# Optimization experiments

Hardware: AMD Instinct MI355X
Metric: run time of the kernel (lower is better)

The kernel has to match this reference:

```python
import jax, jax.numpy as jnp
import numpy as np

B, T_IN, T_OUT, C = 32, 512, 256, 64
NB_IN, NB_OUT = 16, 16
D = 128          # d_model
L = 3            # e_layers (hidden Siren layers before last)
E_IN = NB_IN * C
E_OUT = NB_OUT * C
LIN_IN = (NB_IN + 1) * C + 4
LIN_OUT = (NB_OUT + 1) * C


def _siren_params(key, E, w0_initial):
    ks = jax.random.split(key, 6)
    def unif(k, shape, std):
        return jax.random.uniform(k, shape, jnp.float32, -std, std)
    c6 = float(np.sqrt(6.0 / D))
    return dict(
        W0=unif(ks[0], (E, D, 1), 1.0),        # first layer: w_std = 1/dim_in, dim_in=1
        b0=unif(ks[1], (E, D), 1.0),
        Wh=unif(ks[2], (L - 1, E, D, D), c6),   # sqrt(6/dim)/w0, w0=1
        bh=unif(ks[3], (L - 1, E, D), c6),
        Wl=unif(ks[4], (E, 1, D), c6),
        bl=unif(ks[5], (E, 1), c6),
        w0i=w0_initial,                          # per-ensemble first-layer frequency
    )


def setup_inputs() -> dict:
    key = jax.random.key(0)
    ks = jax.random.split(key, 8)
    inp = {
        "x_enc": jax.random.normal(ks[0], (B, T_IN, C), jnp.float32),
        "x_mark_enc": jax.random.normal(ks[1], (B, T_IN, 4), jnp.float32),
        "x_dec": jax.random.normal(ks[2], (B, T_OUT, C), jnp.float32),
        "x_mark_dec": jax.random.normal(ks[3], (B, T_OUT, 4), jnp.float32),
    }
    # w0_initial: repeat(linspace(1, nb, nb), 'e -> (e c)')
    w0i_in = jnp.repeat(jnp.linspace(1.0, NB_IN, NB_IN, dtype=jnp.float32), C)
    w0i_out = jnp.repeat(jnp.linspace(1.0, NB_OUT, NB_OUT, dtype=jnp.float32), C)
    p_in = _siren_params(ks[4], E_IN, w0i_in)
    p_out = _siren_params(ks[5], E_OUT, w0i_out)
    for k, v in p_in.items():
        inp[k + "_in"] = v
    for k, v in p_out.items():
        inp[k + "_out"] = v
    std = float(1.0 / np.sqrt(LIN_IN))
    inp["Wlin"] = jax.random.uniform(ks[6], (LIN_OUT, LIN_IN), jnp.float32, -std, std)
    inp["blin"] = jax.random.uniform(ks[7], (LIN_OUT,), jnp.float32, -std, std)
    return inp


def _eigenfunc(T, nb, W0, b0, Wh, bh, Wl, bl, w0i):
    # SirenNet on domain [T,1] -> normalized eigenfunctions [T, nb+1, C]
    domain = jnp.linspace(0.0, 1.0, T, dtype=W0.dtype)[:, None]
    y = jnp.einsum('eoi,ti->teo', W0, domain) + b0           # [T,E,D]
    x = jnp.sin(w0i[None, :, None] * y)                       # Sine(w0_initial)
    for l in range(Wh.shape[0]):                              # hidden layers, w0 = 1
        x = jnp.sin(jnp.einsum('eoi,tei->teo', Wh[l], x) + bh[l])
    y = jnp.einsum('eoi,tei->teo', Wl, x) + bl                # [T,E,1], identity final act
    ef = y.reshape(T, nb, C)                                  # 't (e c) 1 -> t e c'
    ef = jnp.concatenate([jnp.ones((T, 1, C), ef.dtype), ef], axis=1)  # add_ones
    norm = jnp.sqrt(jnp.sum(ef * ef, axis=1, keepdims=True))  # normalize over basis dim
    return ef / norm


def reference(x_enc, x_mark_enc, x_dec, x_mark_dec,
              W0_in, b0_in, Wh_in, bh_in, Wl_in, bl_in, w0i_in,
              W0_out, b0_out, Wh_out, bh_out, Wl_out, bl_out, w0i_out,
              Wlin, blin):
    ef_in = _eigenfunc(T_IN, NB_IN, W0_in, b0_in, Wh_in, bh_in, Wl_in, bl_in, w0i_in)
    ef_out = _eigenfunc(T_OUT, NB_OUT, W0_out, b0_out, Wh_out, bh_out, Wl_out, bl_out, w0i_out)
    coeffs = jnp.einsum('btc,tec->bec', x_enc, ef_in)         # [B, nb+1, C]
    label = x_mark_enc[:, -1]                                  # [B, 4]
    flat = coeffs.reshape(coeffs.shape[0], -1)                 # 'b e c -> b (e c)'
    flat_in = jnp.concatenate([flat, label], axis=-1)
    pred = flat_in @ Wlin.T + blin                             # nn.Linear
    pred_coeff = pred.reshape(-1, NB_OUT + 1, C)
    pred_recon = jnp.einsum('bec,tec->btc', pred_coeff, ef_out)  # [B, pred_len, C]
    return pred_recon
```

## Files before the change

### kernel.cpp

```cpp
#include <hip/hip_runtime.h>
#include <hip/hip_bf16.h>
#include <math.h>


typedef short  bf16x8 __attribute__((ext_vector_type(8)));
typedef float  f32x4  __attribute__((ext_vector_type(4)));
typedef unsigned short u16;
typedef u16    u16x8  __attribute__((ext_vector_type(8)));
typedef unsigned int u32;
typedef u32    u32x4  __attribute__((ext_vector_type(4)));

constexpr int DD    = 128;
constexpr int E_TOT = 1024;
constexpr int T_INc = 512;
constexpr int T_OUTc= 256;
constexpr int BBc   = 32;
constexpr int CCc   = 64;
constexpr int NB1   = 17;
constexpr int EF_W  = NB1 * CCc;
constexpr int LIN_I = EF_W + 4;
constexpr int LIN_O = EF_W;

__device__ __forceinline__ u16 f2b(float f) {
  unsigned u = __builtin_bit_cast(unsigned, f);
  return (u16)((u + 0x7FFFu + ((u >> 16) & 1u)) >> 16);
}
__device__ __forceinline__ float b2f(u16 u) {
  unsigned v = ((unsigned)u) << 16;
  return __builtin_bit_cast(float, v);
}
__device__ __forceinline__ u32 pkrn(float a, float b) {
  __hip_bfloat162 h = __float22bfloat162_rn(float2{a, b});
  u32 r;
  __builtin_memcpy(&r, &h, 4);
  return r;
}

__device__ __forceinline__ int swz(int row, int col) {
  return row * DD + ((((col << 1) ^ ((row & 15) << 4)) >> 1));
}

__global__ __launch_bounds__(512, 4) void eigen_persist(
    const float* __restrict__ W0i, const float* __restrict__ b0i,
    const float* __restrict__ Whi, const float* __restrict__ bhi,
    const float* __restrict__ Wli, const float* __restrict__ bli,
    const float* __restrict__ w0ii, float* __restrict__ efni,
    const float* __restrict__ W0o, const float* __restrict__ b0o,
    const float* __restrict__ Who, const float* __restrict__ bho,
    const float* __restrict__ Wlo, const float* __restrict__ blo,
    const float* __restrict__ w0io, float* __restrict__ efno)
{
  __shared__ u16 xP[2][8192];
  __shared__ float w0s[128], b0s[128], wls[128];

  const bool isIn = (blockIdx.x < E_TOT);
  const int  e    = blockIdx.x & (E_TOT - 1);
  const int  NIT  = isIn ? (T_INc / 64) : (T_OUTc / 64);
  const float tstep = isIn ? (1.0f / (float)(T_INc - 1)) : (1.0f / (float)(T_OUTc - 1));
  const float* W0 = isIn ? W0i : W0o;
  const float* b0 = isIn ? b0i : b0o;
  const float* Wh = isIn ? Whi : Who;
  const float* bh = isIn ? bhi : bho;
  const float* Wl = isIn ? Wli : Wlo;
  const float* bl = isIn ? bli : blo;
  const float* w0i = isIn ? w0ii : w0io;
  float* efn = isIn ? efni : efno;

  const int tid  = threadIdx.x;
  const int lane = tid & 63;
  const int wv   = tid >> 6;
  const int wt   = wv >> 2;
  const int wo   = wv & 3;
  const int lm   = lane & 15;
  const int lg   = lane >> 4;

  if (tid < 128)       w0s[tid]       = W0[(size_t)e * DD + tid];
  else if (tid < 256)  b0s[tid - 128] = b0[(size_t)e * DD + tid - 128];
  else if (tid < 384)  wls[tid - 256] = Wl[(size_t)e * DD + tid - 256];
  const float wi  = w0i[e];
  const float blv = bl[e];

  float bhv[2][2];
  #pragma unroll
  for (int l = 0; l < 2; ++l)
    #pragma unroll
    for (int n = 0; n < 2; ++n)
      bhv[l][n] = bh[((size_t)l * E_TOT + e) * DD + wo * 32 + n * 16 + lm];

  bf16x8 wfrag[2][4][2];
  #pragma unroll
  for (int l = 0; l < 2; ++l) {
    const float* Wg = Wh + ((size_t)l * E_TOT + e) * (DD * DD);
    #pragma unroll
    for (int kk = 0; kk < 4; ++kk)
      #pragma unroll
      for (int n = 0; n < 2; ++n) {
        const float* p = Wg + (wo * 32 + n * 16 + lm) * DD + kk * 32 + lg * 8;
        const float4 a = *(const float4*)p;
        const float4 c = *(const float4*)(p + 4);
        u32x4 u;
        u[0] = pkrn(a.x, a.y);
        u[1] = pkrn(a.z, a.w);
        u[2] = pkrn(c.x, c.y);
        u[3] = pkrn(c.z, c.w);
        wfrag[l][kk][n] = __builtin_bit_cast(bf16x8, u);
      }
  }
  __syncthreads();

  const int tl = tid >> 3;
  const int q  = tid & 7;

  for (int it = 0; it < NIT; ++it) {
    u16* pCur = xP[it & 1];
    u16* pAlt = xP[(it & 1) ^ 1];

    {
      const float dom = (float)(it * 64 + tl) * tstep;
      #pragma unroll
      for (int c = 0; c < 2; ++c) {
        const int d = q * 16 + c * 8;
        const float4 wa = *(const float4*)&w0s[d];
        const float4 wb = *(const float4*)&w0s[d + 4];
        const float4 ba = *(const float4*)&b0s[d];
        const float4 bb = *(const float4*)&b0s[d + 4];
        u32x4 u;
        u[0] = pkrn(__sinf(wi * (wa.x * dom + ba.x)), __sinf(wi * (wa.y * dom + ba.y)));
        u[1] = pkrn(__sinf(wi * (wa.z * dom + ba.z)), __sinf(wi * (wa.w * dom + ba.w)));
        u[2] = pkrn(__sinf(wi * (wb.x * dom + bb.x)), __sinf(wi * (wb.y * dom + bb.y)));
        u[3] = pkrn(__sinf(wi * (wb.z * dom + bb.z)), __sinf(wi * (wb.w * dom + bb.w)));
        *(u16x8*)&pCur[swz(tl, d)] = __builtin_bit_cast(u16x8, u);
      }
    }
    __syncthreads();

    f32x4 acc[2][2];

    #pragma unroll
    for (int m = 0; m < 2; ++m)
      #pragma unroll
      for (int n = 0; n < 2; ++n) acc[m][n] = (f32x4){0.f, 0.f, 0.f, 0.f};
    #pragma unroll
    for (int kk = 0; kk < 4; ++kk) {
      const int kb = kk * 32 + lg * 8;
      bf16x8 ah[2];
      #pragma unroll
      for (int m = 0; m < 2; ++m)
        ah[m] = *(const bf16x8*)&pCur[swz(wt * 32 + m * 16 + lm, kb)];
      #pragma unroll
      for (int m = 0; m < 2; ++m)
        #pragma unroll
        for (int n = 0; n < 2; ++n)
          acc[m][n] = __builtin_amdgcn_mfma_f32_16x16x32_bf16(ah[m], wfrag[0][kk][n], acc[m][n], 0, 0, 0);
    }
    #pragma unroll
    for (int m = 0; m < 2; ++m)
      #pragma unroll
      for (int n = 0; n < 2; ++n) {
        const int o = wo * 32 + n * 16 + lm;
        const int t = wt * 32 + m * 16 + lg * 4;
        const u32 p0 = pkrn(__sinf(acc[m][n][0] + bhv[0][n]), __sinf(acc[m][n][1] + bhv[0][n]));
        const u32 p1 = pkrn(__sinf(acc[m][n][2] + bhv[0][n]), __sinf(acc[m][n][3] + bhv[0][n]));
        pAlt[swz(t + 0, o)] = (u16)p0;
        pAlt[swz(t + 1, o)] = (u16)(p0 >> 16);
        pAlt[swz(t + 2, o)] = (u16)p1;
        pAlt[swz(t + 3, o)] = (u16)(p1 >> 16);
      }
    __syncthreads();

    #pragma unroll
    for (int m = 0; m < 2; ++m)
      #pragma unroll
      for (int n = 0; n < 2; ++n) acc[m][n] = (f32x4){0.f, 0.f, 0.f, 0.f};
    #pragma unroll
    for (int kk = 0; kk < 4; ++kk) {
      const int kb = kk * 32 + lg * 8;
      bf16x8 ah[2];
      #pragma unroll
      for (int m = 0; m < 2; ++m)
        ah[m] = *(const bf16x8*)&pAlt[swz(wt * 32 + m * 16 + lm, kb)];
      #pragma unroll
      for (int m = 0; m < 2; ++m)
        #pragma unroll
        for (int n = 0; n < 2; ++n)
          acc[m][n] = __builtin_amdgcn_mfma_f32_16x16x32_bf16(ah[m], wfrag[1][kk][n], acc[m][n], 0, 0, 0);
    }
    #pragma unroll
    for (int m = 0; m < 2; ++m)
      #pragma unroll
      for (int n = 0; n < 2; ++n) {
        const int o = wo * 32 + n * 16 + lm;
        const int t = wt * 32 + m * 16 + lg * 4;
        const u32 p0 = pkrn(__sinf(acc[m][n][0] + bhv[1][n]), __sinf(acc[m][n][1] + bhv[1][n]));
        const u32 p1 = pkrn(__sinf(acc[m][n][2] + bhv[1][n]), __sinf(acc[m][n][3] + bhv[1][n]));
        pCur[swz(t + 0, o)] = (u16)p0;
        pCur[swz(t + 1, o)] = (u16)(p0 >> 16);
        pCur[swz(t + 2, o)] = (u16)p1;
        pCur[swz(t + 3, o)] = (u16)(p1 >> 16);
      }
    __syncthreads();

    {
      const int i = q * 16;
      float a = 0.0f;
      const bf16x8 h0 = *(const bf16x8*)&pCur[swz(tl, i)];
      const bf16x8 h1 = *(const bf16x8*)&pCur[swz(tl, i + 8)];
      const float4 wl0 = *(const float4*)&wls[i];
      const float4 wl1 = *(const float4*)&wls[i + 4];
      const float4 wl2 = *(const float4*)&wls[i + 8];
      const float4 wl3 = *(const float4*)&wls[i + 12];
      a += wl0.x * b2f((u16)h0[0]) + wl0.y * b2f((u16)h0[1])
         + wl0.z * b2f((u16)h0[2]) + wl0.w * b2f((u16)h0[3]);
      a += wl1.x * b2f((u16)h0[4]) + wl1.y * b2f((u16)h0[5])
         + wl1.z * b2f((u16)h0[6]) + wl1.w * b2f((u16)h0[7]);
      a += wl2.x * b2f((u16)h1[0]) + wl2.y * b2f((u16)h1[1])
         + wl2.z * b2f((u16)h1[2]) + wl2.w * b2f((u16)h1[3]);
      a += wl3.x * b2f((u16)h1[4]) + wl3.y * b2f((u16)h1[5])
         + wl3.z * b2f((u16)h1[6]) + wl3.w * b2f((u16)h1[7]);
      a += __shfl_xor(a, 1);
      a += __shfl_xor(a, 2);
      a += __shfl_xor(a, 4);
      if (q == 0)
        efn[(size_t)(it * 64 + tl) * EF_W + CCc + e] = a + blv;
    }
  }
}

__global__ void normalize_kernel(float* __restrict__ efn)
{
  const int t = blockIdx.x;
  const int c = threadIdx.x;
  float* row = efn + (size_t)t * EF_W;
  float v[16];
  float s = 1.0f;
  #pragma unroll
  for (int n = 0; n < 16; ++n) {
    v[n] = row[CCc + n * CCc + c];
    s += v[n] * v[n];
  }
  const float inv = 1.0f / sqrtf(s);
  row[c] = inv;
  #pragma unroll
  for (int n = 0; n < 16; ++n)
    row[CCc + n * CCc + c] = v[n] * inv;
}

__global__ __launch_bounds__(512) void coeffs_kernel(
    const float* __restrict__ x_enc, const float* __restrict__ x_mark_enc,
    const float* __restrict__ efn_in, float* __restrict__ flat_in)
{
  const int n  = blockIdx.x;
  const int b  = blockIdx.y;
  const int c  = threadIdx.x & 63;
  const int ch = threadIdx.x >> 6;
  __shared__ float red[8][64];
  float acc = 0.0f;
  #pragma unroll 4
  for (int t = ch * 64; t < ch * 64 + 64; ++t)
    acc += x_enc[((size_t)b * T_INc + t) * CCc + c]
         * efn_in[(size_t)t * EF_W + n * CCc + c];
  red[ch][c] = acc;
  __syncthreads();
  if (ch == 0) {
    #pragma unroll
    for (int k = 1; k < 8; ++k) acc += red[k][c];
    flat_in[b * LIN_I + n * CCc + c] = acc;
    if (n == 0 && c < 4)
      flat_in[b * LIN_I + EF_W + c] =
          x_mark_enc[((size_t)b * T_INc + (T_INc - 1)) * 4 + c];
  }
}

__global__ __launch_bounds__(256) void transpose_lin(const float* __restrict__ W,
                                                     float* __restrict__ Wt)
{
  __shared__ float tile[32][33];
  const int j0 = blockIdx.x * 32;
  const int o0 = blockIdx.y * 32;
  const int tx = threadIdx.x & 31, ty = threadIdx.x >> 5;
  #pragma unroll
  for (int r = 0; r < 32; r += 8) {
    const int o = o0 + ty + r, j = j0 + tx;
    tile[ty + r][tx] = (o < LIN_O && j < LIN_I) ? W[(size_t)o * LIN_I + j] : 0.f;
  }
  __syncthreads();
  #pragma unroll
  for (int r = 0; r < 32; r += 8) {
    const int j = j0 + ty + r, o = o0 + tx;
    if (j < LIN_I && o < LIN_O) Wt[(size_t)j * LIN_O + o] = tile[tx][ty + r];
  }
}

__global__ __launch_bounds__(256) void linear_t_kernel(
    const float* __restrict__ flat_in, const float* __restrict__ Wt,
    const float* __restrict__ blin, float* __restrict__ pred)
{
  const int og = blockIdx.x;
  const int b  = blockIdx.y;
  const int c  = threadIdx.x & 63;
  const int ch = threadIdx.x >> 6;
  const int o  = og * 64 + c;
  __shared__ float red[4][64];
  const float* xi = flat_in + b * LIN_I;
  float acc = 0.0f;
  #pragma unroll 4
  for (int j = ch * 273; j < ch * 273 + 273; ++j)
    acc += Wt[(size_t)j * LIN_O + o] * xi[j];
  red[ch][c] = acc;
  __syncthreads();
  if (ch == 0)
    pred[b * LIN_O + o] = acc + red[1][c] + red[2][c] + red[3][c] + blin[o];
}

__global__ void linear_row_kernel(const float* __restrict__ flat_in,
                                  const float* __restrict__ Wlin,
                                  const float* __restrict__ blin,
                                  float* __restrict__ pred)
{
  const int o = blockIdx.x * 64 + threadIdx.x;
  const int b = blockIdx.y;
  const float* w  = Wlin + (size_t)o * LIN_I;
  const float* xi = flat_in + b * LIN_I;
  float acc = blin[o];
  for (int j = 0; j < LIN_I; ++j) acc += w[j] * xi[j];
  pred[b * LIN_O + o] = acc;
}

__global__ void recon_kernel(const float* __restrict__ pred,
                             const float* __restrict__ efn_out,
                             float* __restrict__ out)
{
  const int b = blockIdx.y;
  const int t = blockIdx.x * 4 + (threadIdx.x >> 6);
  const int c = threadIdx.x & 63;
  float acc = 0.0f;
  #pragma unroll
  for (int n = 0; n < NB1; ++n)
    acc += pred[b * LIN_O + n * CCc + c]
         * efn_out[(size_t)t * EF_W + n * CCc + c];
  out[((size_t)b * T_OUTc + t) * CCc + c] = acc;
}

extern "C" void kernel_launch(void* const* d_in, const int* in_sizes, int n_in,
                              void* d_out, int out_size, void* d_ws, size_t ws_size,
                              hipStream_t stream)
{
  const float* x_enc      = (const float*)d_in[0];
  const float* x_mark_enc = (const float*)d_in[1];
  const float* W0_in  = (const float*)d_in[4];
  const float* b0_in  = (const float*)d_in[5];
  const float* Wh_in  = (const float*)d_in[6];
  const float* bh_in  = (const float*)d_in[7];
  const float* Wl_in  = (const float*)d_in[8];
  const float* bl_in  = (const float*)d_in[9];
  const float* w0i_in = (const float*)d_in[10];
  const float* W0_out  = (const float*)d_in[11];
  const float* b0_out  = (const float*)d_in[12];
  const float* Wh_out  = (const float*)d_in[13];
  const float* bh_out  = (const float*)d_in[14];
  const float* Wl_out  = (const float*)d_in[15];
  const float* bl_out  = (const float*)d_in[16];
  const float* w0i_out = (const float*)d_in[17];
  const float* Wlin = (const float*)d_in[18];
  const float* blin = (const float*)d_in[19];

  float* ws      = (float*)d_ws;
  float* efn_in  = ws;
  float* efn_out = efn_in + (size_t)T_INc * EF_W;
  float* flat_in = efn_out + (size_t)T_OUTc * EF_W;
  float* pred    = flat_in + (size_t)BBc * LIN_I;
  float* Wt      = pred + (size_t)BBc * LIN_O;
  const size_t needWt = ((size_t)(Wt - ws) + (size_t)LIN_I * LIN_O) * sizeof(float);
  const bool useWt = (ws_size >= needWt);

  eigen_persist<<<dim3(2 * E_TOT), dim3(512), 0, stream>>>(
      W0_in, b0_in, Wh_in, bh_in, Wl_in, bl_in, w0i_in, efn_in,
      W0_out, b0_out, Wh_out, bh_out, Wl_out, bl_out, w0i_out, efn_out);

  normalize_kernel<<<dim3(T_INc),  dim3(64), 0, stream>>>(efn_in);
  normalize_kernel<<<dim3(T_OUTc), dim3(64), 0, stream>>>(efn_out);

  coeffs_kernel<<<dim3(NB1, BBc), dim3(512), 0, stream>>>(x_enc, x_mark_enc, efn_in, flat_in);

  if (useWt) {
    transpose_lin<<<dim3((LIN_I + 31) / 32, (LIN_O + 31) / 32), dim3(256), 0, stream>>>(Wlin, Wt);
    linear_t_kernel<<<dim3(NB1, BBc), dim3(256), 0, stream>>>(flat_in, Wt, blin, pred);
  } else {
    linear_row_kernel<<<dim3(NB1, BBc), dim3(64), 0, stream>>>(flat_in, Wlin, blin, pred);
  }

  recon_kernel<<<dim3(T_OUTc / 4, BBc), dim3(256), 0, stream>>>(pred, efn_out, (float*)d_out);
}
```

Before: 205.4 us.

## Transpose MFMA operands and fuse final Siren layer dot into register epilogue

Swaps the MFMA operand roles so the weights are the A operand and activations the B operand. Accumulator rows now map to contiguous output features, which lets the first hidden layer store packed 8-byte LDS writes instead of scalar 16-bit ones. The second hidden layer's sine and the final linear dot with Wl are computed directly from the accumulators, reduced with shuffles and a small LDS partial array, which drops one LDS round trip. It also changes the swizzle pattern and lowers the launch-bounds occupancy hint from 4 to 2, which may alter register allocation and occupancy.

Result: slower. 235.0 us (+14.4%).

```diff
diff --git a/kernel.cpp b/kernel.cpp
--- a/kernel.cpp
+++ b/kernel.cpp
@@ -8,6 +8,7 @@
 typedef unsigned short u16;
 typedef u16    u16x8  __attribute__((ext_vector_type(8)));
 typedef unsigned int u32;
+typedef u32    u32x2  __attribute__((ext_vector_type(2)));
 typedef u32    u32x4  __attribute__((ext_vector_type(4)));
 
 constexpr int DD    = 128;
@@ -21,10 +22,6 @@
 constexpr int LIN_I = EF_W + 4;
 constexpr int LIN_O = EF_W;
 
-__device__ __forceinline__ u16 f2b(float f) {
-  unsigned u = __builtin_bit_cast(unsigned, f);
-  return (u16)((u + 0x7FFFu + ((u >> 16) & 1u)) >> 16);
-}
 __device__ __forceinline__ float b2f(u16 u) {
   unsigned v = ((unsigned)u) << 16;
   return __builtin_bit_cast(float, v);
@@ -37,10 +34,10 @@
 }
 
 __device__ __forceinline__ int swz(int row, int col) {
-  return row * DD + ((((col << 1) ^ ((row & 15) << 4)) >> 1));
-}
-
-__global__ __launch_bounds__(512, 4) void eigen_persist(
+  return row * DD + ((((col << 1) ^ ((row & 7) << 4)) >> 1));
+}
+
+__global__ __launch_bounds__(512, 2) void eigen_persist(
     const float* __restrict__ W0i, const float* __restrict__ b0i,
     const float* __restrict__ Whi, const float* __restrict__ bhi,
     const float* __restrict__ Wli, const float* __restrict__ bli,
@@ -51,7 +48,8 @@
     const float* __restrict__ w0io, float* __restrict__ efno)
 {
   __shared__ u16 xP[2][8192];
-  __shared__ float w0s[128], b0s[128], wls[128];
+  __shared__ float yPart[4 * 64];
+  __shared__ float w0s[128], b0s[128];
 
   const bool isIn = (blockIdx.x < E_TOT);
   const int  e    = blockIdx.x & (E_TOT - 1);
@@ -76,16 +74,17 @@
 
   if (tid < 128)       w0s[tid]       = W0[(size_t)e * DD + tid];
   else if (tid < 256)  b0s[tid - 128] = b0[(size_t)e * DD + tid - 128];
-  else if (tid < 384)  wls[tid - 256] = Wl[(size_t)e * DD + tid - 256];
   const float wi  = w0i[e];
   const float blv = bl[e];
 
-  float bhv[2][2];
-  #pragma unroll
-  for (int l = 0; l < 2; ++l)
-    #pragma unroll
-    for (int n = 0; n < 2; ++n)
-      bhv[l][n] = bh[((size_t)l * E_TOT + e) * DD + wo * 32 + n * 16 + lm];
+  float4 bh1v[2], bh2v[2], wlv[2];
+  #pragma unroll
+  for (int m = 0; m < 2; ++m) {
+    const int ob = wo * 32 + m * 16 + lg * 4;
+    bh1v[m] = *(const float4*)(bh + (size_t)e * DD + ob);
+    bh2v[m] = *(const float4*)(bh + ((size_t)E_TOT + e) * DD + ob);
+    wlv[m]  = *(const float4*)(Wl + (size_t)e * DD + ob);
+  }
 
   bf16x8 wfrag[2][4][2];
   #pragma unroll
@@ -94,8 +93,8 @@
     #pragma unroll
     for (int kk = 0; kk < 4; ++kk)
       #pragma unroll
-      for (int n = 0; n < 2; ++n) {
-        const float* p = Wg + (wo * 32 + n * 16 + lm) * DD + kk * 32 + lg * 8;
+      for (int m = 0; m < 2; ++m) {
+        const float* p = Wg + (wo * 32 + m * 16 + lm) * DD + kk * 32 + lg * 8;
         const float4 a = *(const float4*)p;
         const float4 c = *(const float4*)(p + 4);
         u32x4 u;
@@ -103,7 +102,7 @@
         u[1] = pkrn(a.z, a.w);
         u[2] = pkrn(c.x, c.y);
         u[3] = pkrn(c.z, c.w);
-        wfrag[l][kk][n] = __builtin_bit_cast(bf16x8, u);
+        wfrag[l][kk][m] = __builtin_bit_cast(bf16x8, u);
       }
   }
   __syncthreads();
@@ -112,8 +111,8 @@
   const int q  = tid & 7;
 
   for (int it = 0; it < NIT; ++it) {
-    u16* pCur = xP[it & 1];
-    u16* pAlt = xP[(it & 1) ^ 1];
+    u16* x0p = xP[0];
+    u16* x1p = xP[1];
 
     {
       const float dom = (float)(it * 64 + tl) * tstep;
@@ -129,7 +128,7 @@
         u[1] = pkrn(__sinf(wi * (wa.z * dom + ba.z)), __sinf(wi * (wa.w * dom + ba.w)));
         u[2] = pkrn(__sinf(wi * (wb.x * dom + bb.x)), __sinf(wi * (wb.y * dom + bb.y)));
         u[3] = pkrn(__sinf(wi * (wb.z * dom + bb.z)), __sinf(wi * (wb.w * dom + bb.w)));
-        *(u16x8*)&pCur[swz(tl, d)] = __builtin_bit_cast(u16x8, u);
+        *(u16x8*)&x0p[swz(tl, d)] = __builtin_bit_cast(u16x8, u);
       }
     }
     __syncthreads();
@@ -143,28 +142,26 @@
     #pragma unroll
     for (int kk = 0; kk < 4; ++kk) {
       const int kb = kk * 32 + lg * 8;
-      bf16x8 ah[2];
-      #pragma unroll
-      for (int m = 0; m < 2; ++m)
-        ah[m] = *(const bf16x8*)&pCur[swz(wt * 32 + m * 16 + lm, kb)];
+      bf16x8 xf[2];
+      #pragma unroll
+      for (int n = 0; n < 2; ++n)
+        xf[n] = *(const bf16x8*)&x0p[swz(wt * 32 + n * 16 + lm, kb)];
       #pragma unroll
       for (int m = 0; m < 2; ++m)
         #pragma unroll
         for (int n = 0; n < 2; ++n)
-          acc[m][n] = __builtin_amdgcn_mfma_f32_16x16x32_bf16(ah[m], wfrag[0][kk][n], acc[m][n], 0, 0, 0);
+          acc[m][n] = __builtin_amdgcn_mfma_f32_16x16x32_bf16(wfrag[0][kk][m], xf[n], acc[m][n], 0, 0, 0);
     }
     #pragma unroll
     for (int m = 0; m < 2; ++m)
       #pragma unroll
       for (int n = 0; n < 2; ++n) {
-        const int o = wo * 32 + n * 16 + lm;
-        const int t = wt * 32 + m * 16 + lg * 4;
-        const u32 p0 = pkrn(__sinf(acc[m][n][0] + bhv[0][n]), __sinf(acc[m][n][1] + bhv[0][n]));
-        const u32 p1 = pkrn(__sinf(acc[m][n][2] + bhv[0][n]), __sinf(acc[m][n][3] + bhv[0][n]));
-        pAlt[swz(t + 0, o)] = (u16)p0;
-        pAlt[swz(t + 1, o)] = (u16)(p0 >> 16);
-        pAlt[swz(t + 2, o)] = (u16)p1;
-        pAlt[swz(t + 3, o)] = (u16)(p1 >> 16);
+        const int t  = wt * 32 + n * 16 + lm;
+        const int ob = wo * 32 + m * 16 + lg * 4;
+        u32x2 w2;
+        w2[0] = pkrn(__sinf(acc[m][n][0] + bh1v[m].x), __sinf(acc[m][n][1] + bh1v[m].y));
+        w2[1] = pkrn(__sinf(acc[m][n][2] + bh1v[m].z), __sinf(acc[m][n][3] + bh1v[m].w));
+        *(u32x2*)&x1p[swz(t, ob)] = w2;
       }
     __syncthreads();
 
@@ -175,53 +172,41 @@
     #pragma unroll
     for (int kk = 0; kk < 4; ++kk) {
       const int kb = kk * 32 + lg * 8;
-      bf16x8 ah[2];
-      #pragma unroll
-      for (int m = 0; m < 2; ++m)
-        ah[m] = *(const bf16x8*)&pAlt[swz(wt * 32 + m * 16 + lm, kb)];
+      bf16x8 xf[2];
+      #pragma unroll
+      for (int n = 0; n < 2; ++n)
+        xf[n] = *(const bf16x8*)&x1p[swz(wt * 32 + n * 16 + lm, kb)];
       #pragma unroll
       for (int m = 0; m < 2; ++m)
         #pragma unroll
         for (int n = 0; n < 2; ++n)
-          acc[m][n] = __builtin_amdgcn_mfma_f32_16x16x32_bf16(ah[m], wfrag[1][kk][n], acc[m][n], 0, 0, 0);
-    }
-    #pragma unroll
-    for (int m = 0; m < 2; ++m)
-      #pragma unroll
-      for (int n = 0; n < 2; ++n) {
-        const int o = wo * 32 + n * 16 + lm;
-        const int t = wt * 32 + m * 16 + lg * 4;
-        const u32 p0 = pkrn(__sinf(acc[m][n][0] + bhv[1][n]), __sinf(acc[m][n][1] + bhv[1][n]));
-        const u32 p1 = pkrn(__sinf(acc[m][n][2] + bhv[1][n]), __sinf(acc[m][n][3] + bhv[1][n]));
-        pCur[swz(t + 0, o)] = (u16)p0;
-        pCur[swz(t + 1, o)] = (u16)(p0 >> 16);
-        pCur[swz(t + 2, o)] = (u16)p1;
-        pCur[swz(t + 3, o)] = (u16)(p1 >> 16);
-      }
+          acc[m][n] = __builtin_amdgcn_mfma_f32_16x16x32_bf16(wfrag[1][kk][m], xf[n], acc[m][n], 0, 0, 0);
+    }
+
+    {
+      float part0 = 0.f, part1 = 0.f;
+      #pragma unroll
+      for (int m = 0; m < 2; ++m) {
+        const float* bp = (const float*)&bh2v[m];
+        const float* wp = (const float*)&wlv[m];
+        #pragma unroll
+        for (int r = 0; r < 4; ++r) {
+          part0 += wp[r] * __sinf(acc[m][0][r] + bp[r]);
+          part1 += wp[r] * __sinf(acc[m][1][r] + bp[r]);
+        }
+      }
+      part0 += __shfl_xor(part0, 16);  part0 += __shfl_xor(part0, 32);
+      part1 += __shfl_xor(part1, 16);  part1 += __shfl_xor(part1, 32);
+      if (lg == 0) {
+        yPart[wo * 64 + wt * 32 + lm]      = part0;
+        yPart[wo * 64 + wt * 32 + 16 + lm] = part1;
+      }
+    }
     __syncthreads();
 
-    {
-      const int i = q * 16;
-      float a = 0.0f;
-      const bf16x8 h0 = *(const bf16x8*)&pCur[swz(tl, i)];
-      const bf16x8 h1 = *(const bf16x8*)&pCur[swz(tl, i + 8)];
-      const float4 wl0 = *(const float4*)&wls[i];
-      const float4 wl1 = *(const float4*)&wls[i + 4];
-      const float4 wl2 = *(const float4*)&wls[i + 8];
-      const float4 wl3 = *(const float4*)&wls[i + 12];
-      a += wl0.x * b2f((u16)h0[0]) + wl0.y * b2f((u16)h0[1])
-         + wl0.z * b2f((u16)h0[2]) + wl0.w * b2f((u16)h0[3]);
-      a += wl1.x * b2f((u16)h0[4]) + wl1.y * b2f((u16)h0[5])
-         + wl1.z * b2f((u16)h0[6]) + wl1.w * b2f((u16)h0[7]);
-      a += wl2.x * b2f((u16)h1[0]) + wl2.y * b2f((u16)h1[1])
-         + wl2.z * b2f((u16)h1[2]) + wl2.w * b2f((u16)h1[3]);
-      a += wl3.x * b2f((u16)h1[4]) + wl3.y * b2f((u16)h1[5])
-         + wl3.z * b2f((u16)h1[6]) + wl3.w * b2f((u16)h1[7]);
-      a += __shfl_xor(a, 1);
-      a += __shfl_xor(a, 2);
-      a += __shfl_xor(a, 4);
-      if (q == 0)
-        efn[(size_t)(it * 64 + tl) * EF_W + CCc + e] = a + blv;
+    if (tid < 64) {
+      const float s = yPart[tid] + yPart[64 + tid] + yPart[128 + tid] + yPart[192 + tid];
+      efn[(size_t)(it * 64 + tid) * EF_W + CCc + e] = s + blv;
     }
   }
 }
```
